# Performance work log

Hardware: AMD Instinct MI355X
Metric: run time of the kernel (lower is better)

The kernel has to match this reference:

```python
import jax, jax.numpy as jnp
import numpy as np

SIZE = 4096


def setup_inputs() -> dict:
    key = jax.random.key(0)
    npars = SIZE * (SIZE - 1) // 2
    unconst_params = jax.random.normal(key, (npars,), dtype=jnp.float32)
    return {"unconst_params": unconst_params, "size": SIZE}


def _chol_fac(unconst_params, size):
    # Scatter tanh(params) into the strict lower triangle of z.
    ri, ci = np.tril_indices(size, -1)  # static indices
    z = jnp.zeros((size, size), unconst_params.dtype)
    z = z.at[ri, ci].set(jnp.tanh(unconst_params))
    # Closed form of the row recurrence:
    #   s_0 = 1,  x[i,j] = z[i,j]*sqrt(s_j),  s_{j+1} = s_j*(1 - z[i,j]^2)
    # => x[i,j] = z[i,j] * sqrt(prod_{k<j}(1 - z[i,k]^2)), diag uses z=1.
    one_minus = 1.0 - z * z  # equals 1 outside strict lower triangle
    cp = jnp.cumprod(one_minus, axis=1)
    # exclusive cumprod along columns: s_j = prod_{k<j}(1 - z[i,k]^2)
    s = jnp.concatenate([jnp.ones((size, 1), z.dtype), cp[:, :-1]], axis=1)
    # z + I puts the implicit z=1 on the diagonal; upper triangle stays 0.
    x = (z + jnp.eye(size, dtype=z.dtype)) * jnp.sqrt(s)
    return x


def reference(unconst_params, size):
    lmat = _chol_fac(unconst_params, size)  # [size, size] lower triangular
    return lmat @ lmat.T  # correlation matrix, unit diagonal
```

## Files before the change

### kernel.cpp

```cpp
#include <hip/hip_runtime.h>
#include <hip/hip_bf16.h>

#define SIZE 4096
#define BM 256
#define BK 64
#define NT (SIZE / BK)
#define NBG (SIZE / BM)

typedef __bf16 bf16x8 __attribute__((ext_vector_type(8)));
typedef __bf16 bf16x4 __attribute__((ext_vector_type(4)));
typedef float f32x4 __attribute__((ext_vector_type(4)));
typedef float f32x16 __attribute__((ext_vector_type(16)));

__device__ __forceinline__ void gload_lds16(const void* gsrc, void* ldst) {
  __builtin_amdgcn_global_load_lds(
      (const __attribute__((address_space(1))) unsigned int*)gsrc,
      (__attribute__((address_space(3))) unsigned int*)ldst, 16, 0, 0);
}

__global__ __launch_bounds__(256) void build_L(const float* __restrict__ p,
                                               __bf16* __restrict__ Lb) {
  const int row = blockIdx.x;
  const int tid = threadIdx.x;
  const int lane = tid & 63;
  const int wid = tid >> 6;
  const long base = (long)row * (row - 1) / 2;

  __shared__ float wtot[4];
  float carry = 1.0f;

  for (int j0 = 0; j0 < SIZE; j0 += 1024) {
    const int jb = j0 + tid * 4;
    if (j0 > row) {
      bf16x4 z = {(__bf16)0.0f, (__bf16)0.0f, (__bf16)0.0f, (__bf16)0.0f};
      *(bf16x4*)&Lb[(size_t)row * SIZE + jb] = z;
      continue;
    }
    float t[4], v[4];
#pragma unroll
    for (int e = 0; e < 4; ++e) {
      const int j = jb + e;
      if (j < row) {
        const float th = tanhf(p[base + j]);
        t[e] = th;
        v[e] = 1.0f - th * th;
      } else {
        t[e] = (j == row) ? 1.0f : 0.0f;
        v[e] = 1.0f;
      }
    }
    const float vt = v[0] * v[1] * v[2] * v[3];
    float incl = vt;
#pragma unroll
    for (int off = 1; off < 64; off <<= 1) {
      float o = __shfl_up(incl, off, 64);
      if (lane >= off) incl *= o;
    }
    if (lane == 63) wtot[wid] = incl;
    __syncthreads();
    float pre = carry;
    for (int w = 0; w < wid; ++w) pre *= wtot[w];
    float excl = __shfl_up(incl, 1, 64);
    if (lane == 0) excl = 1.0f;
    float s = pre * excl;
    bf16x4 out;
#pragma unroll
    for (int e = 0; e < 4; ++e) {
      out[e] = (__bf16)(t[e] * sqrtf(s));
      s *= v[e];
    }
    *(bf16x4*)&Lb[(size_t)row * SIZE + jb] = out;
    const float tot = wtot[0] * wtot[1] * wtot[2] * wtot[3];
    __syncthreads();
    carry *= tot;
  }
}

__global__ __launch_bounds__(512, 1) void syrk8(const __bf16* __restrict__ Lb,
                                                float* __restrict__ C) {
  __shared__ __bf16 lds[2][2][2][256][32];

  const int bid0 = blockIdx.x;
  const int bid = (bid0 & 7) * 32 + (bid0 >> 3);
  const int bi = bid >> 4, bj = bid & 15;

  const int tid = threadIdx.x;
  const int lane = tid & 63;
  const int wid = tid >> 6;
  const int wm = wid >> 2;
  const int wn = wid & 3;
  const int r32 = lane & 31;
  const int khi = lane >> 5;
  const int swzf = ((r32 >> 1) & 3) ^ ((lane >> 4) & 1);
  const int ck0 = ((0 | khi) ^ swzf) * 8;
  const int ck1 = ((2 | khi) ^ swzf) * 8;

  const size_t rowA0 = (size_t)bi * 256;
  const size_t rowB0 = (size_t)bj * 256;

  const int srow = wid * 32 + (lane >> 2);
  const int sch = (lane & 3) ^ ((lane >> 3) & 3);
  const int soff0 = sch * 8;
  const int soff1 = (sch ^ 1) * 8;

  const __bf16* g0 = Lb + (rowA0 + srow) * SIZE;
  const __bf16* g1 = Lb + (rowB0 + srow) * SIZE;
  const __bf16* g2 = Lb + (rowA0 + srow) * SIZE + 32;
  const __bf16* g3 = Lb + (rowB0 + srow) * SIZE + 32;

  auto stg = [&](const __bf16*& gp, int ab, int kh, int dstbuf) {
    __bf16* base = &lds[dstbuf][ab][kh][0][0];
    gload_lds16(gp + soff0, base + (wid * 32) * 32);
    gload_lds16(gp + (size_t)16 * SIZE + soff1, base + (wid * 32 + 16) * 32);
    gp += BK;
  };

  f32x16 acc[4][2] = {};

  stg(g0, 0, 0, 0); stg(g1, 1, 0, 0); stg(g2, 0, 1, 0); stg(g3, 1, 1, 0);
  stg(g0, 0, 0, 1); stg(g1, 1, 0, 1); stg(g2, 0, 1, 1);
  asm volatile("s_waitcnt vmcnt(6)" ::: "memory");
  __builtin_amdgcn_s_barrier();

  for (int t = 0; t < NT; ++t) {
    const int buf = t & 1, nbuf = buf ^ 1;
    bf16x8 af[2][2], bf[2][2];
#pragma unroll
    for (int i = 0; i < 4; ++i) {
      const int kh = i >> 1, mh = i & 1;
      if (mh == 0) {
#pragma unroll
        for (int nb = 0; nb < 2; ++nb) {
          const __bf16* bp = &lds[buf][1][kh][wn * 64 + nb * 32 + r32][0];
          bf[nb][0] = *(const bf16x8*)(bp + ck0);
          bf[nb][1] = *(const bf16x8*)(bp + ck1);
        }
      }
#pragma unroll
      for (int mb = 0; mb < 2; ++mb) {
        const __bf16* ap =
            &lds[buf][0][kh][wm * 128 + (mh * 2 + mb) * 32 + r32][0];
        af[mb][0] = *(const bf16x8*)(ap + ck0);
        af[mb][1] = *(const bf16x8*)(ap + ck1);
      }

      if (i == 0)      { if (t < NT - 1) stg(g3, 1, 1, nbuf); }
      else if (i == 1) { if (t < NT - 2) stg(g0, 0, 0, buf); }
      else if (i == 2) { if (t < NT - 2) stg(g1, 1, 0, buf); }
      else             { if (t < NT - 2) stg(g2, 0, 1, buf); }

      if (i == 3) {
        if (t == NT - 2)
          asm volatile("s_waitcnt vmcnt(0)" ::: "memory");
        else if (t < NT - 2)
          asm volatile("s_waitcnt vmcnt(6)" ::: "memory");
      }
      __builtin_amdgcn_s_barrier();
      asm volatile("s_waitcnt lgkmcnt(0)" ::: "memory");
      __builtin_amdgcn_sched_barrier(0);
      __builtin_amdgcn_s_setprio(1);
#pragma unroll
      for (int mb = 0; mb < 2; ++mb)
#pragma unroll
        for (int nb = 0; nb < 2; ++nb)
#pragma unroll
          for (int ks = 0; ks < 2; ++ks)
            acc[mh * 2 + mb][nb] = __builtin_amdgcn_mfma_f32_32x32x16_bf16(
                af[mb][ks], bf[nb][ks], acc[mh * 2 + mb][nb], 0, 0, 0);
      __builtin_amdgcn_s_setprio(0);
      __builtin_amdgcn_s_barrier();
    }
  }

  float* Cp = C + (rowA0 + wm * 128) * (size_t)SIZE + rowB0 + wn * 64;
#pragma unroll
  for (int mb = 0; mb < 4; ++mb)
#pragma unroll
    for (int nb = 0; nb < 2; ++nb)
#pragma unroll
      for (int j = 0; j < 16; ++j)
        Cp[(size_t)(mb * 32 + (j & 3) + 8 * (j >> 2) + 4 * khi) * SIZE +
           nb * 32 + r32] = acc[mb][nb][j];
}

extern "C" void kernel_launch(void* const* d_in, const int* in_sizes, int n_in,
                              void* d_out, int out_size, void* d_ws, size_t ws_size,
                              hipStream_t stream) {
  const float* p = (const float*)d_in[0];
  float* C = (float*)d_out;
  __bf16* Lb = (__bf16*)d_ws;

  build_L<<<SIZE, 256, 0, stream>>>(p, Lb);
  syrk8<<<NBG * NBG, 512, 0, stream>>>(Lb, C);
}
```

Before: 134.1 us.

## Double-buffer LDS fragment registers to overlap reads with MFMA in syrk

Restructures the syrk main loop so LDS fragment loads for the next quarter-step go into a second register set while MFMAs run on the current one. It waits with lgkmcnt(8) instead of draining all LDS reads before each MFMA group. It also reorders the global-to-LDS staging sequence and prefetches the first fragments before the loop. This hides LDS latency behind matrix math, at the cost of more registers and a more delicate staging/barrier order.

```diff
diff --git a/kernel.cpp b/kernel.cpp
--- a/kernel.cpp
+++ b/kernel.cpp
@@ -116,60 +116,79 @@
   };
 
   f32x16 acc[4][2] = {};
+  bf16x8 afA[2][2], bfA[2][2], afB[2][2], bfB[2][2];
+
+#define LDRD(AF, BF, BSEL, KH, MH)                                         \
+  {                                                                        \
+    _Pragma("unroll") for (int mb = 0; mb < 2; ++mb) {                     \
+      const __bf16* ap =                                                   \
+          &lds[BSEL][0][KH][wm * 128 + ((MH)*2 + mb) * 32 + r32][0];       \
+      AF[mb][0] = *(const bf16x8*)(ap + ck0);                              \
+      AF[mb][1] = *(const bf16x8*)(ap + ck1);                              \
+    }                                                                      \
+    _Pragma("unroll") for (int nb = 0; nb < 2; ++nb) {                     \
+      const __bf16* bp = &lds[BSEL][1][KH][wn * 64 + nb * 32 + r32][0];    \
+      BF[nb][0] = *(const bf16x8*)(bp + ck0);                              \
+      BF[nb][1] = *(const bf16x8*)(bp + ck1);                              \
+    }                                                                      \
+  }
+
+#define MMA(AF, BF, MH)                                                    \
+  {                                                                        \
+    __builtin_amdgcn_s_setprio(1);                                         \
+    _Pragma("unroll") for (int mb = 0; mb < 2; ++mb)                       \
+        _Pragma("unroll") for (int nb = 0; nb < 2; ++nb)                   \
+            _Pragma("unroll") for (int ks = 0; ks < 2; ++ks)               \
+                acc[(MH)*2 + mb][nb] =                                     \
+        __builtin_amdgcn_mfma_f32_32x32x16_bf16(AF[mb][ks], BF[nb][ks],    \
+                                                acc[(MH)*2 + mb][nb], 0,   \
+                                                0, 0);                     \
+    __builtin_amdgcn_s_setprio(0);                                         \
+  }
+
+#define LGKM8 asm volatile("s_waitcnt lgkmcnt(8)" ::: "memory");           \
+  __builtin_amdgcn_sched_barrier(0)
+#define LGKM0 asm volatile("s_waitcnt lgkmcnt(0)" ::: "memory");           \
+  __builtin_amdgcn_sched_barrier(0)
 
   stg(g0, 0, 0, 0); stg(g1, 1, 0, 0); stg(g2, 0, 1, 0); stg(g3, 1, 1, 0);
-  stg(g0, 0, 0, 1); stg(g1, 1, 0, 1); stg(g2, 0, 1, 1);
+  stg(g1, 1, 0, 1); stg(g0, 0, 0, 1); stg(g3, 1, 1, 1);
   asm volatile("s_waitcnt vmcnt(6)" ::: "memory");
   __builtin_amdgcn_s_barrier();
+  LDRD(afA, bfA, 0, 0, 0);
 
   for (int t = 0; t < NT; ++t) {
     const int buf = t & 1, nbuf = buf ^ 1;
-    bf16x8 af[2][2], bf[2][2];
-#pragma unroll
-    for (int i = 0; i < 4; ++i) {
-      const int kh = i >> 1, mh = i & 1;
-      if (mh == 0) {
-#pragma unroll
-        for (int nb = 0; nb < 2; ++nb) {
-          const __bf16* bp = &lds[buf][1][kh][wn * 64 + nb * 32 + r32][0];
-          bf[nb][0] = *(const bf16x8*)(bp + ck0);
-          bf[nb][1] = *(const bf16x8*)(bp + ck1);
-        }
-      }
-#pragma unroll
-      for (int mb = 0; mb < 2; ++mb) {
-        const __bf16* ap =
-            &lds[buf][0][kh][wm * 128 + (mh * 2 + mb) * 32 + r32][0];
-        af[mb][0] = *(const bf16x8*)(ap + ck0);
-        af[mb][1] = *(const bf16x8*)(ap + ck1);
-      }
-
-      if (i == 0)      { if (t < NT - 1) stg(g3, 1, 1, nbuf); }
-      else if (i == 1) { if (t < NT - 2) stg(g0, 0, 0, buf); }
-      else if (i == 2) { if (t < NT - 2) stg(g1, 1, 0, buf); }
-      else             { if (t < NT - 2) stg(g2, 0, 1, buf); }
-
-      if (i == 3) {
-        if (t == NT - 2)
-          asm volatile("s_waitcnt vmcnt(0)" ::: "memory");
-        else if (t < NT - 2)
-          asm volatile("s_waitcnt vmcnt(6)" ::: "memory");
-      }
-      __builtin_amdgcn_s_barrier();
-      asm volatile("s_waitcnt lgkmcnt(0)" ::: "memory");
-      __builtin_amdgcn_sched_barrier(0);
-      __builtin_amdgcn_s_setprio(1);
-#pragma unroll
-      for (int mb = 0; mb < 2; ++mb)
-#pragma unroll
-        for (int nb = 0; nb < 2; ++nb)
-#pragma unroll
-          for (int ks = 0; ks < 2; ++ks)
-            acc[mh * 2 + mb][nb] = __builtin_amdgcn_mfma_f32_32x32x16_bf16(
-                af[mb][ks], bf[nb][ks], acc[mh * 2 + mb][nb], 0, 0, 0);
-      __builtin_amdgcn_s_setprio(0);
-      __builtin_amdgcn_s_barrier();
-    }
+    if (t < NT - 1) stg(g2, 0, 1, nbuf);
+    LDRD(afB, bfB, buf, 0, 1);
+    LGKM8;
+    MMA(afA, bfA, 0);
+    __builtin_amdgcn_s_barrier();
+    if (t < NT - 2) stg(g1, 1, 0, buf);
+    LDRD(afA, bfA, buf, 1, 0);
+    LGKM8;
+    MMA(afB, bfB, 1);
+    __builtin_amdgcn_s_barrier();
+    if (t < NT - 2) stg(g0, 0, 0, buf);
+    LDRD(afB, bfB, buf, 1, 1);
+    LGKM8;
+    MMA(afA, bfA, 0);
+    __builtin_amdgcn_s_barrier();
+    if (t < NT - 2) {
+      stg(g3, 1, 1, buf);
+      asm volatile("s_waitcnt vmcnt(6)" ::: "memory");
+    } else if (t == NT - 2) {
+      asm volatile("s_waitcnt vmcnt(0)" ::: "memory");
+    }
+    __builtin_amdgcn_s_barrier();
+    if (t < NT - 1) {
+      LDRD(afA, bfA, nbuf, 0, 0);
+      LGKM8;
+    } else {
+      LGKM0;
+    }
+    MMA(afB, bfB, 1);
+    __builtin_amdgcn_s_barrier();
   }
 
   float* Cp = C + (rowA0 + wm * 128) * (size_t)SIZE + rowB0 + wn * 64;
@@ -181,6 +200,10 @@
       for (int j = 0; j < 16; ++j)
         Cp[(size_t)(mb * 32 + (j & 3) + 8 * (j >> 2) + 4 * khi) * SIZE +
            nb * 32 + r32] = acc[mb][nb][j];
+#undef LDRD
+#undef MMA
+#undef LGKM8
+#undef LGKM0
 }
 
 extern "C" void kernel_launch(void* const* d_in, const int* in_sizes, int n_in,
```

Measured after the change: 134.8 us. No clear change (+0.5%).
